# Kernel tuning notes

Hardware: AMD Instinct MI355X
Metric: run time of the kernel (lower is better)

Reference implementation:

```python
import jax, jax.numpy as jnp
import numpy as np

B, T, E = 64, 64, 256
S, ENC = 128, 1024
RNN, ATT, DENSE = 1024, 1024, 8000


def setup_inputs() -> dict:
    key = jax.random.key(0)
    ks = jax.random.split(key, 16)
    s = 0.02
    return {
        "initial_input": jax.random.normal(ks[0], (B, T, E), jnp.float32),
        "hidden": jax.random.normal(ks[1], (B, RNN), jnp.float32),
        "cell": jax.random.normal(ks[2], (B, RNN), jnp.float32),
        "encoder_output": jax.random.normal(ks[3], (B, S, ENC), jnp.float32),
        "W1": jax.random.normal(ks[4], (RNN, ATT), jnp.float32) * s,
        "b1": jnp.zeros((ATT,), jnp.float32),
        "W2": jax.random.normal(ks[5], (ENC, ATT), jnp.float32) * s,
        "b2": jnp.zeros((ATT,), jnp.float32),
        "V": jax.random.normal(ks[6], (ATT, 1), jnp.float32) * s,
        "bV": jnp.zeros((1,), jnp.float32),
        "kernel": jax.random.normal(ks[7], (ENC + E, 4 * RNN), jnp.float32) * s,
        "rkernel": jax.random.normal(ks[8], (RNN, 4 * RNN), jnp.float32) * s,
        "bias": jnp.zeros((4 * RNN,), jnp.float32),
        "Wd": jax.random.normal(ks[9], (RNN, DENSE), jnp.float32) * s,
        "bd": jnp.zeros((DENSE,), jnp.float32),
        "seq_len": T,
    }


def _decode(initial_input, hidden, cell, encoder_output,
            W1, b1, W2, b2, V, bV, kernel, rkernel, bias, Wd, bd):
    # Keys W2(encoder_output) are step-independent: precompute once. [B,S,ATT]
    keys = jnp.einsum('bse,ea->bsa', encoder_output, W2) + b2

    def step(carry, x_t):
        h, c = carry
        # Bahdanau attention: score = V^T tanh(W1 h + W2 enc)
        q = h @ W1 + b1                                  # [B,ATT]
        score = jnp.tanh(q[:, None, :] + keys) @ V + bV   # [B,S,1]
        attn = jax.nn.softmax(score, axis=1)              # [B,S,1]
        ctx = jnp.sum(attn * encoder_output, axis=1)      # [B,ENC]
        # LSTM cell (Keras gate order i,f,g,o; sigmoid/tanh activations)
        inp = jnp.concatenate([ctx, x_t], axis=-1)        # [B,ENC+E]
        z = inp @ kernel + h @ rkernel + bias              # [B,4*RNN]
        i, f, g, o = jnp.split(z, 4, axis=-1)
        i = jax.nn.sigmoid(i)
        f = jax.nn.sigmoid(f)
        g = jnp.tanh(g)
        o = jax.nn.sigmoid(o)
        c_new = f * c + i * g
        h_new = o * jnp.tanh(c_new)
        logits = h_new @ Wd + bd                           # [B,DENSE]
        return (h_new, c_new), logits

    xs = jnp.swapaxes(initial_input, 0, 1)  # [T,B,E]
    (h, c), logits = jax.lax.scan(step, (hidden, cell), xs)
    outputs = jnp.swapaxes(logits, 0, 1)    # [B,T,DENSE]
    return outputs, h, c


def reference(initial_input, hidden, cell, encoder_output,
              W1, b1, W2, b2, V, bV, kernel, rkernel, bias, Wd, bd, seq_len):
    # seq_len == initial_input.shape[1] (static); the Python loop in the
    # original is expressed as an efficient lax.scan over decode steps.
    return _decode(initial_input[:, :seq_len, :], hidden, cell, encoder_output,
                   W1, b1, W2, b2, V, bV, kernel, rkernel, bias, Wd, bd)
```

## Files before the change

### kernel.cpp

```cpp
#include <hip/hip_runtime.h>
#include <hip/hip_bf16.h>
#include <stdint.h>


typedef __attribute__((ext_vector_type(8))) short short8;
typedef __attribute__((ext_vector_type(4))) float floatx4;
typedef __attribute__((ext_vector_type(4))) unsigned short ushortx4;

__device__ __forceinline__ float b2f(unsigned short u) {
    union { unsigned int i; float f; } v; v.i = ((unsigned int)u) << 16; return v.f;
}
__device__ __forceinline__ unsigned short f2b(float f) {
    union { float f; unsigned int i; } v; v.f = f;
    unsigned int r = v.i + 0x7fffu + ((v.i >> 16) & 1u);
    return (unsigned short)(r >> 16);
}
__device__ __forceinline__ float ftanh(float x) {
    x = fminf(15.f, fmaxf(-15.f, x));
    float e = __expf(2.f * x);
    return (e - 1.f) * __builtin_amdgcn_rcpf(e + 1.f);
}
__device__ __forceinline__ float fsig(float x) {
    return __builtin_amdgcn_rcpf(1.f + __expf(-x));
}
__device__ __forceinline__ void ld_lds16(const void* g, void* l) {
    __builtin_amdgcn_global_load_lds((const __attribute__((address_space(1))) void*)g,
                                     (__attribute__((address_space(3))) void*)l, 16, 0, 0);
}

__global__ __launch_bounds__(256) void conv_f32_bf16(
    const float* __restrict__ src, unsigned short* __restrict__ dst, int n4)
{
    int i = blockIdx.x * 256 + threadIdx.x;
    if (i < n4) {
        float4 v = ((const float4*)src)[i];
        ushortx4 o;
        o[0] = f2b(v.x); o[1] = f2b(v.y); o[2] = f2b(v.z); o[3] = f2b(v.w);
        ((ushortx4*)dst)[i] = o;
    }
}

__global__ __launch_bounds__(256) void transpose_conv(
    const float* __restrict__ src, int srcld,
    unsigned short* __restrict__ dst, int dstld, int coloff, int perm)
{
    __shared__ float tile[32][33];
    const int k0 = blockIdx.y * 32, n0 = blockIdx.x * 32;
    const int r = threadIdx.x >> 3, c = (threadIdx.x & 7) * 4;
    int n = n0 + c;
    int cn = perm ? ((((n >> 4) & 3) << 10) | ((n >> 6) << 4) | (n & 15)) : n;
    float4 v = *(const float4*)&src[(size_t)(k0 + r) * srcld + cn];
    tile[r][c + 0] = v.x; tile[r][c + 1] = v.y;
    tile[r][c + 2] = v.z; tile[r][c + 3] = v.w;
    __syncthreads();
    const int nr = threadIdx.x >> 3, kc = (threadIdx.x & 7) * 4;
    ushortx4 o;
    o[0] = f2b(tile[kc + 0][nr]);
    o[1] = f2b(tile[kc + 1][nr]);
    o[2] = f2b(tile[kc + 2][nr]);
    o[3] = f2b(tile[kc + 3][nr]);
    *(ushortx4*)&dst[(size_t)(n0 + nr) * dstld + coloff + k0 + kc] = o;
}

__global__ __launch_bounds__(256) void gemm_bf16_128(
    const unsigned short* __restrict__ A, int lda,
    const unsigned short* __restrict__ BT, int ldbt, int K,
    float* __restrict__ Cf, unsigned short* __restrict__ Cb,
    int ldc, int ncols, const float* __restrict__ bias)
{
    __shared__ __align__(16) unsigned short As[128 * 32];
    __shared__ __align__(16) unsigned short Bs[128 * 32];
    const int tid = threadIdx.x, wave = tid >> 6, lane = tid & 63;
    const int q = lane >> 4, lm = lane & 15;
    const int wr = wave >> 1, wc = wave & 1;
    const int m0 = blockIdx.y * 128, n0 = blockIdx.x * 128;
    const int srow = lane >> 2;
    const int gch = (lane & 3) ^ ((lane >> 3) & 3);
    const unsigned short* Ag0 = A + (size_t)(m0 + wave * 32 + srow) * lda + gch * 8;
    const unsigned short* Ag1 = Ag0 + (size_t)16 * lda;
    const unsigned short* Bg0 = BT + (size_t)(n0 + wave * 32 + srow) * ldbt + gch * 8;
    const unsigned short* Bg1 = Bg0 + (size_t)16 * ldbt;
    unsigned short* Al0 = &As[(wave * 32) * 32];
    unsigned short* Al1 = &As[(wave * 32 + 16) * 32];
    unsigned short* Bl0 = &Bs[(wave * 32) * 32];
    unsigned short* Bl1 = &Bs[(wave * 32 + 16) * 32];

    const floatx4 z4 = {0.f, 0.f, 0.f, 0.f};
    floatx4 acc[4][4];
#pragma unroll
    for (int i = 0; i < 4; i++)
#pragma unroll
        for (int j = 0; j < 4; j++) acc[i][j] = z4;
    const int ach = ((q ^ ((lm >> 1) & 3))) * 8;

    for (int kb = 0; kb < K; kb += 32) {
        ld_lds16(Ag0 + kb, Al0);
        ld_lds16(Ag1 + kb, Al1);
        ld_lds16(Bg0 + kb, Bl0);
        ld_lds16(Bg1 + kb, Bl1);
        __syncthreads();
        short8 a[4], b[4];
#pragma unroll
        for (int i = 0; i < 4; i++) a[i] = *(const short8*)&As[(wr * 64 + i * 16 + lm) * 32 + ach];
#pragma unroll
        for (int j = 0; j < 4; j++) b[j] = *(const short8*)&Bs[(wc * 64 + j * 16 + lm) * 32 + ach];
#pragma unroll
        for (int i = 0; i < 4; i++)
#pragma unroll
            for (int j = 0; j < 4; j++)
                acc[i][j] = __builtin_amdgcn_mfma_f32_16x16x32_bf16(a[i], b[j], acc[i][j], 0, 0, 0);
        __syncthreads();
    }
    const int rb = m0 + wr * 64 + q * 4;
#pragma unroll
    for (int i = 0; i < 4; i++) {
#pragma unroll
        for (int j = 0; j < 4; j++) {
            int col = n0 + wc * 64 + j * 16 + lm;
            if (col < ncols) {
                float bv = bias ? bias[col] : 0.f;
#pragma unroll
                for (int r = 0; r < 4; r++) {
                    float v = acc[i][j][r] + bv;
                    size_t idx = (size_t)(rb + i * 16 + r) * ldc + col;
                    if (Cf) Cf[idx] = v;
                    if (Cb) Cb[idx] = f2b(v);
                }
            }
        }
    }
}

__global__ __launch_bounds__(256) void gemm64_split(
    const unsigned short* __restrict__ A, int lda,
    const unsigned short* __restrict__ BT, int ldbt,
    int kchunk, float* __restrict__ Cpart, int ldc)
{
    __shared__ __align__(16) unsigned short As[4][64 * 32];
    __shared__ __align__(16) unsigned short Bs[4][64 * 32];
    const int tid = threadIdx.x, wave = tid >> 6, lane = tid & 63;
    const int q = lane >> 4, lm = lane & 15;
    const int n0 = blockIdx.x * 64;
    const int k0 = blockIdx.z * kchunk;
    const int srow = lane >> 2;
    const int gch = (lane & 3) ^ ((lane >> 3) & 3);
    const unsigned short* Ag = A + (size_t)(wave * 16 + srow) * lda + k0 + gch * 8;
    const unsigned short* Bg = BT + (size_t)(n0 + wave * 16 + srow) * ldbt + k0 + gch * 8;
    const int loff = (wave * 16) * 32;
    const floatx4 z4 = {0.f, 0.f, 0.f, 0.f};
    floatx4 acc0 = z4, acc1 = z4, acc2 = z4, acc3 = z4;
    const int ach = ((q ^ ((lm >> 1) & 3))) * 8;
    const int nit = kchunk >> 5;

#pragma unroll
    for (int p = 0; p < 3; ++p) {
        if (p < nit) {
            ld_lds16(Ag + p * 32, &As[p][loff]);
            ld_lds16(Bg + p * 32, &Bs[p][loff]);
        }
    }
    for (int it = 0; it < nit; ++it) {
        const int st = it & 3;
        if (it + 2 < nit)      asm volatile("s_waitcnt vmcnt(4)\n\ts_barrier" ::: "memory");
        else if (it + 1 < nit) asm volatile("s_waitcnt vmcnt(2)\n\ts_barrier" ::: "memory");
        else                   asm volatile("s_waitcnt vmcnt(0)\n\ts_barrier" ::: "memory");
        if (it + 3 < nit) {
            const int sn = (it + 3) & 3;
            ld_lds16(Ag + (it + 3) * 32, &As[sn][loff]);
            ld_lds16(Bg + (it + 3) * 32, &Bs[sn][loff]);
        }
        short8 a  = *(const short8*)&As[st][(wave * 16 + lm) * 32 + ach];
        short8 b0 = *(const short8*)&Bs[st][(0 * 16 + lm) * 32 + ach];
        short8 b1 = *(const short8*)&Bs[st][(1 * 16 + lm) * 32 + ach];
        short8 b2 = *(const short8*)&Bs[st][(2 * 16 + lm) * 32 + ach];
        short8 b3 = *(const short8*)&Bs[st][(3 * 16 + lm) * 32 + ach];
        acc0 = __builtin_amdgcn_mfma_f32_16x16x32_bf16(a, b0, acc0, 0, 0, 0);
        acc1 = __builtin_amdgcn_mfma_f32_16x16x32_bf16(a, b1, acc1, 0, 0, 0);
        acc2 = __builtin_amdgcn_mfma_f32_16x16x32_bf16(a, b2, acc2, 0, 0, 0);
        acc3 = __builtin_amdgcn_mfma_f32_16x16x32_bf16(a, b3, acc3, 0, 0, 0);
    }
    float* Cp = Cpart + (size_t)blockIdx.z * 64 * ldc;
    const int rb = wave * 16 + q * 4;
    floatx4 accs[4] = {acc0, acc1, acc2, acc3};
#pragma unroll
    for (int i = 0; i < 4; i++) {
        int col = n0 + i * 16 + lm;
#pragma unroll
        for (int r = 0; r < 4; r++) Cp[(size_t)(rb + r) * ldc + col] = accs[i][r];
    }
}

__global__ __launch_bounds__(256) void init_hc(
    const float* __restrict__ hidden, const float* __restrict__ cell,
    float* __restrict__ hf, float* __restrict__ cb, unsigned short* __restrict__ hbf)
{
    int idx = blockIdx.x * 256 + threadIdx.x;
    float h = hidden[idx], c = cell[idx];
    hf[idx] = h; cb[idx] = c; hbf[idx] = f2b(h);
}

__global__ __launch_bounds__(256) void attn_scores(
    const float* __restrict__ qp, const float* __restrict__ b1,
    const unsigned short* __restrict__ keys,
    const float* __restrict__ V, const float* __restrict__ bV,
    float* __restrict__ sc)
{
    __shared__ float qs[1024];
    __shared__ float vs[1024];
    const int b = blockIdx.y, sg = blockIdx.x;
    const int tid = threadIdx.x, wave = tid >> 6, lane = tid & 63;
    {
        float4 a0 = ((const float4*)(qp + (size_t)b * 1024))[tid];
        float4 a1 = ((const float4*)(qp + 65536 + (size_t)b * 1024))[tid];
        float4 a2 = ((const float4*)(qp + 131072 + (size_t)b * 1024))[tid];
        float4 a3 = ((const float4*)(qp + 196608 + (size_t)b * 1024))[tid];
        float4 ab = ((const float4*)b1)[tid];
        float4 av = ((const float4*)V)[tid];
        float4 r;
        r.x = a0.x + a1.x + a2.x + a3.x + ab.x;
        r.y = a0.y + a1.y + a2.y + a3.y + ab.y;
        r.z = a0.z + a1.z + a2.z + a3.z + ab.z;
        r.w = a0.w + a1.w + a2.w + a3.w + ab.w;
        *(float4*)&qs[tid * 4] = r;
        *(float4*)&vs[tid * 4] = av;
    }
    __syncthreads();
    float qr[16], vr[16];
#pragma unroll
    for (int i = 0; i < 4; i++) {
        float4 tq = *(const float4*)&qs[lane * 16 + i * 4];
        float4 tv = *(const float4*)&vs[lane * 16 + i * 4];
        qr[i * 4 + 0] = tq.x; qr[i * 4 + 1] = tq.y; qr[i * 4 + 2] = tq.z; qr[i * 4 + 3] = tq.w;
        vr[i * 4 + 0] = tv.x; vr[i * 4 + 1] = tv.y; vr[i * 4 + 2] = tv.z; vr[i * 4 + 3] = tv.w;
    }
    const float bv0 = bV[0];
#pragma unroll
    for (int i = 0; i < 4; i++) {
        const int s = sg * 16 + wave * 4 + i;
        const uint4* kp = (const uint4*)(keys + ((size_t)(b * 128 + s)) * 1024 + lane * 16);
        uint4 k0 = kp[0], k1 = kp[1];
        float kf[16];
        kf[0] = b2f((unsigned short)(k0.x & 0xffff)); kf[1] = b2f((unsigned short)(k0.x >> 16));
        kf[2] = b2f((unsigned short)(k0.y & 0xffff)); kf[3] = b2f((unsigned short)(k0.y >> 16));
        kf[4] = b2f((unsigned short)(k0.z & 0xffff)); kf[5] = b2f((unsigned short)(k0.z >> 16));
        kf[6] = b2f((unsigned short)(k0.w & 0xffff)); kf[7] = b2f((unsigned short)(k0.w >> 16));
        kf[8] = b2f((unsigned short)(k1.x & 0xffff)); kf[9] = b2f((unsigned short)(k1.x >> 16));
        kf[10] = b2f((unsigned short)(k1.y & 0xffff)); kf[11] = b2f((unsigned short)(k1.y >> 16));
        kf[12] = b2f((unsigned short)(k1.z & 0xffff)); kf[13] = b2f((unsigned short)(k1.z >> 16));
        kf[14] = b2f((unsigned short)(k1.w & 0xffff)); kf[15] = b2f((unsigned short)(k1.w >> 16));
        float part = 0.f;
#pragma unroll
        for (int j = 0; j < 16; j++) part += vr[j] * ftanh(qr[j] + kf[j]);
#pragma unroll
        for (int off = 32; off; off >>= 1) part += __shfl_xor(part, off);
        if (lane == 0) sc[b * 128 + s] = part + bv0;
    }
}

__global__ __launch_bounds__(256) void softmax_ctx(
    const float* __restrict__ sc, const unsigned short* __restrict__ enc_bf,
    const float* __restrict__ x, const unsigned short* __restrict__ hbf,
    unsigned short* __restrict__ Axc, int t)
{
    __shared__ float attnv[128];
    __shared__ float red[4][64][2];
    __shared__ float smax_s, ssum_s;
    const int b = blockIdx.y, chunk = blockIdx.x;
    const int tid = threadIdx.x, wave = tid >> 6, lane = tid & 63;
    float sv = 0.f;
    if (tid < 128) { sv = sc[b * 128 + tid]; attnv[tid] = sv; }
    __syncthreads();
    if (tid < 64) {
        float m = fmaxf(attnv[tid], attnv[tid + 64]);
#pragma unroll
        for (int off = 32; off; off >>= 1) m = fmaxf(m, __shfl_xor(m, off));
        if (tid == 0) smax_s = m;
    }
    __syncthreads();
    if (tid < 128) attnv[tid] = __expf(sv - smax_s);
    __syncthreads();
    if (tid < 64) {
        float s2 = attnv[tid] + attnv[tid + 64];
#pragma unroll
        for (int off = 32; off; off >>= 1) s2 += __shfl_xor(s2, off);
        if (tid == 0) ssum_s = s2;
    }
    if (chunk < 2 && tid < 64) {
        int c2 = chunk * 128 + tid * 2;
        float x0 = x[((size_t)b * 64 + t) * 256 + c2];
        float x1 = x[((size_t)b * 64 + t) * 256 + c2 + 1];
        *(unsigned int*)&Axc[b * 2304 + 1024 + c2] =
            (unsigned int)f2b(x0) | ((unsigned int)f2b(x1) << 16);
    }
    if (tid < 64) {
        int c2 = chunk * 128 + tid * 2;
        *(unsigned int*)&Axc[b * 2304 + 1280 + c2] =
            *(const unsigned int*)&hbf[b * 1024 + c2];
    }
    const unsigned int* ep = (const unsigned int*)enc_bf + (size_t)b * 65536 + chunk * 64 + lane;
    __syncthreads();
    float ax = 0.f, ay = 0.f;
#pragma unroll 8
    for (int i = 0; i < 32; i++) {
        int s = wave * 32 + i;
        float a = attnv[s];
        unsigned int u = ep[(size_t)s * 512];
        ax += a * b2f((unsigned short)(u & 0xffff));
        ay += a * b2f((unsigned short)(u >> 16));
    }
    red[wave][lane][0] = ax; red[wave][lane][1] = ay;
    __syncthreads();
    if (tid < 64) {
        float rs = __builtin_amdgcn_rcpf(ssum_s);
        float fx = (red[0][lane][0] + red[1][lane][0] + red[2][lane][0] + red[3][lane][0]) * rs;
        float fy = (red[0][lane][1] + red[1][lane][1] + red[2][lane][1] + red[3][lane][1]) * rs;
        *(unsigned int*)&Axc[b * 2304 + chunk * 128 + lane * 2] =
            (unsigned int)f2b(fx) | ((unsigned int)f2b(fy) << 16);
    }
}

__global__ __launch_bounds__(512) void gemm_gates(
    const unsigned short* __restrict__ Axc,
    const unsigned short* __restrict__ KRT,
    const float* __restrict__ bz,
    float* __restrict__ cb, float* __restrict__ hf,
    unsigned short* __restrict__ hbf, unsigned short* __restrict__ Hall, int t)
{
    __shared__ __align__(16) char smem[65536];
    unsigned short* As = (unsigned short*)smem;
    unsigned short* Bs = (unsigned short*)(smem + 32768);
    float* red = (float*)smem;
    const int tid = threadIdx.x, wave = tid >> 6, lane = tid & 63;
    const int q = lane >> 4, lm = lane & 15;
    const int h = wave >> 2, wm = wave & 3;
    const int bx = blockIdx.x;
    const int srow = lane >> 2;
    const int gch = (lane & 3) ^ ((lane >> 3) & 3);
    const unsigned short* Ag = Axc + (size_t)(wm * 16 + srow) * 2304 + h * 1152 + gch * 8;
    const unsigned short* Bg = KRT + (size_t)(bx * 64 + wm * 16 + srow) * 2304 + h * 1152 + gch * 8;
    const int tileoff = h * 2048;
    const int ldoff = tileoff + (wm * 16) * 32;
    const floatx4 z4 = {0.f, 0.f, 0.f, 0.f};
    floatx4 acc0 = z4, acc1 = z4, acc2 = z4, acc3 = z4;
    const int ach = ((q ^ ((lm >> 1) & 3))) * 8;

#pragma unroll
    for (int p = 0; p < 3; ++p) {
        ld_lds16(Ag + p * 32, &As[p * 4096 + ldoff]);
        ld_lds16(Bg + p * 32, &Bs[p * 4096 + ldoff]);
    }
    for (int it = 0; it < 36; ++it) {
        const int st = it & 3;
        if (it < 34)       asm volatile("s_waitcnt vmcnt(4)\n\ts_barrier" ::: "memory");
        else if (it == 34) asm volatile("s_waitcnt vmcnt(2)\n\ts_barrier" ::: "memory");
        else               asm volatile("s_waitcnt vmcnt(0)\n\ts_barrier" ::: "memory");
        if (it + 3 < 36) {
            const int sn = (it + 3) & 3;
            ld_lds16(Ag + (it + 3) * 32, &As[sn * 4096 + ldoff]);
            ld_lds16(Bg + (it + 3) * 32, &Bs[sn * 4096 + ldoff]);
        }
        const unsigned short* Ast = &As[st * 4096 + tileoff];
        const unsigned short* Bst = &Bs[st * 4096 + tileoff];
        short8 a  = *(const short8*)&Ast[(wm * 16 + lm) * 32 + ach];
        short8 b0 = *(const short8*)&Bst[(0 * 16 + lm) * 32 + ach];
        short8 b1 = *(const short8*)&Bst[(1 * 16 + lm) * 32 + ach];
        short8 b2 = *(const short8*)&Bst[(2 * 16 + lm) * 32 + ach];
        short8 b3 = *(const short8*)&Bst[(3 * 16 + lm) * 32 + ach];
        acc0 = __builtin_amdgcn_mfma_f32_16x16x32_bf16(a, b0, acc0, 0, 0, 0);
        acc1 = __builtin_amdgcn_mfma_f32_16x16x32_bf16(a, b1, acc1, 0, 0, 0);
        acc2 = __builtin_amdgcn_mfma_f32_16x16x32_bf16(a, b2, acc2, 0, 0, 0);
        acc3 = __builtin_amdgcn_mfma_f32_16x16x32_bf16(a, b3, acc3, 0, 0, 0);
    }
    __syncthreads();
    if (h == 1) {
        float* rp = &red[(wm * 64 + lane) * 16];
        *(floatx4*)&rp[0]  = acc0; *(floatx4*)&rp[4]  = acc1;
        *(floatx4*)&rp[8]  = acc2; *(floatx4*)&rp[12] = acc3;
    }
    __syncthreads();
    if (h == 0) {
        const float* rp = &red[(wm * 64 + lane) * 16];
        acc0 += *(const floatx4*)&rp[0];
        acc1 += *(const floatx4*)&rp[4];
        acc2 += *(const floatx4*)&rp[8];
        acc3 += *(const floatx4*)&rp[12];
        const int col = bx * 16 + lm;
        const float bzi = bz[col], bzf = bz[1024 + col];
        const float bzg = bz[2048 + col], bzo = bz[3072 + col];
#pragma unroll
        for (int r = 0; r < 4; ++r) {
            const int b = wm * 16 + q * 4 + r;
            float zi = acc0[r] + bzi;
            float zf = acc1[r] + bzf;
            float zg = acc2[r] + bzg;
            float zo = acc3[r] + bzo;
            float ii = fsig(zi), ff = fsig(zf), gg = ftanh(zg), oo = fsig(zo);
            const int idx = b * 1024 + col;
            float cn = ff * cb[idx] + ii * gg;
            float hn = oo * ftanh(cn);
            cb[idx] = cn; hf[idx] = hn;
            unsigned short hb = f2b(hn);
            hbf[idx] = hb;
            Hall[((size_t)b * 64 + t) * 1024 + col] = hb;
        }
    }
}

__global__ __launch_bounds__(256) void tail_k(
    const float* __restrict__ hf, const float* __restrict__ cb, float* __restrict__ out)
{
    int i = blockIdx.x * 256 + threadIdx.x;
    if (i < 65536) out[32768000 + i] = hf[i];
    else out[32768000 + i] = cb[i - 65536];
}

extern "C" void kernel_launch(void* const* d_in, const int* in_sizes, int n_in,
                              void* d_out, int out_size, void* d_ws, size_t ws_size,
                              hipStream_t stream)
{
    const float* x      = (const float*)d_in[0];
    const float* hidden = (const float*)d_in[1];
    const float* cell   = (const float*)d_in[2];
    const float* enc    = (const float*)d_in[3];
    const float* W1     = (const float*)d_in[4];
    const float* b1     = (const float*)d_in[5];
    const float* W2     = (const float*)d_in[6];
    const float* b2     = (const float*)d_in[7];
    const float* V      = (const float*)d_in[8];
    const float* bV     = (const float*)d_in[9];
    const float* Wk     = (const float*)d_in[10];
    const float* rk     = (const float*)d_in[11];
    const float* bz     = (const float*)d_in[12];
    const float* Wd     = (const float*)d_in[13];
    const float* bd     = (const float*)d_in[14];
    float* out = (float*)d_out;

    char* ws = (char*)d_ws;
    unsigned short* enc_bf  = (unsigned short*)(ws + 0);
    unsigned short* keys_bf = (unsigned short*)(ws + 16777216);
    unsigned short* W1T     = (unsigned short*)(ws + 33554432);
    unsigned short* KRT     = (unsigned short*)(ws + 35651584);
    unsigned short* WdT     = (unsigned short*)(ws + 54525952);
    unsigned short* Hall    = (unsigned short*)(ws + 71041024);
    unsigned short* W2T     = Hall;
    unsigned short* Axc     = (unsigned short*)(ws + 79429632);
    float* qp    = (float*)(ws + 79724544);
    float* scbuf = (float*)(ws + 80773120);
    unsigned short* hbf     = (unsigned short*)(ws + 80805888);
    float* hf    = (float*)(ws + 80936960);
    float* cb    = (float*)(ws + 81199104);

    conv_f32_bf16<<<8192, 256, 0, stream>>>(enc, enc_bf, 8388608 / 4);
    transpose_conv<<<dim3(32, 32),  256, 0, stream>>>(W2, 1024, W2T, 1024, 0, 0);
    transpose_conv<<<dim3(32, 32),  256, 0, stream>>>(W1, 1024, W1T, 1024, 0, 0);
    transpose_conv<<<dim3(128, 32), 256, 0, stream>>>(Wk, 4096, KRT, 2304, 0, 1);
    transpose_conv<<<dim3(128, 8),  256, 0, stream>>>(Wk + 1024 * 4096, 4096, KRT, 2304, 1024, 1);
    transpose_conv<<<dim3(128, 32), 256, 0, stream>>>(rk, 4096, KRT, 2304, 1280, 1);
    transpose_conv<<<dim3(250, 32), 256, 0, stream>>>(Wd, 8000, WdT, 1024, 0, 0);
    init_hc<<<256, 256, 0, stream>>>(hidden, cell, hf, cb, hbf);

    gemm_bf16_128<<<dim3(8, 64), 256, 0, stream>>>(enc_bf, 1024, W2T, 1024, 1024,
                                                   nullptr, keys_bf, 1024, 1024, b2);

    for (int t = 0; t < 64; t++) {
        gemm64_split<<<dim3(16, 1, 4), 256, 0, stream>>>(hbf, 1024, W1T, 1024, 256, qp, 1024);
        attn_scores<<<dim3(8, 64), 256, 0, stream>>>(qp, b1, keys_bf, V, bV, scbuf);
        softmax_ctx<<<dim3(8, 64), 256, 0, stream>>>(scbuf, enc_bf, x, hbf, Axc, t);
        gemm_gates<<<64, 512, 0, stream>>>(Axc, KRT, bz, cb, hf, hbf, Hall, t);
    }

    gemm_bf16_128<<<dim3(63, 32), 256, 0, stream>>>(Hall, 1024, WdT, 1024, 1024,
                                                    out, nullptr, 8000, 8000, bd);
    tail_k<<<512, 256, 0, stream>>>(hf, cb, out);
}
```

Before: 2.372 ms.

## Merge prep kernels, fold final state write, swizzle output GEMM, cheaper tanh

Replaces the separate conversion, transpose and init launches with one prep_all kernel indexed by block ID, so there are fewer launches. The final h/c write moves into the last gates step, which removes the tail kernel and the hf buffer. The output GEMM gets an XCD-aware block swizzle so tiles sharing the same A rows land on the same chiplet cache, and its grid grows to 64 columns (relying on the existing ncols guard). The attention tanh switches to a 1-2/(e+1) form with no clamp, which saves a few instructions but could change how extreme inputs are handled.

New measurement: 2.344 ms. No clear change (-1.2%).

```diff
diff --git a/kernel.cpp b/kernel.cpp
--- a/kernel.cpp
+++ b/kernel.cpp
@@ -20,6 +20,9 @@
     float e = __expf(2.f * x);
     return (e - 1.f) * __builtin_amdgcn_rcpf(e + 1.f);
 }
+__device__ __forceinline__ float vtanh(float x) {
+    return __builtin_fmaf(-2.f, __builtin_amdgcn_rcpf(__expf(2.f * x) + 1.f), 1.f);
+}
 __device__ __forceinline__ float fsig(float x) {
     return __builtin_amdgcn_rcpf(1.f + __expf(-x));
 }
@@ -28,32 +31,20 @@
                                      (__attribute__((address_space(3))) void*)l, 16, 0, 0);
 }
 
-__global__ __launch_bounds__(256) void conv_f32_bf16(
-    const float* __restrict__ src, unsigned short* __restrict__ dst, int n4)
-{
-    int i = blockIdx.x * 256 + threadIdx.x;
-    if (i < n4) {
-        float4 v = ((const float4*)src)[i];
-        ushortx4 o;
-        o[0] = f2b(v.x); o[1] = f2b(v.y); o[2] = f2b(v.z); o[3] = f2b(v.w);
-        ((ushortx4*)dst)[i] = o;
-    }
-}
-
-__global__ __launch_bounds__(256) void transpose_conv(
-    const float* __restrict__ src, int srcld,
-    unsigned short* __restrict__ dst, int dstld, int coloff, int perm)
-{
-    __shared__ float tile[32][33];
-    const int k0 = blockIdx.y * 32, n0 = blockIdx.x * 32;
-    const int r = threadIdx.x >> 3, c = (threadIdx.x & 7) * 4;
+__device__ __forceinline__ void tr_tile(
+    float (*tile)[33], const float* __restrict__ src, int srcld,
+    unsigned short* __restrict__ dst, int dstld, int coloff, int perm,
+    int bx, int by, int tid)
+{
+    const int k0 = by * 32, n0 = bx * 32;
+    const int r = tid >> 3, c = (tid & 7) * 4;
     int n = n0 + c;
     int cn = perm ? ((((n >> 4) & 3) << 10) | ((n >> 6) << 4) | (n & 15)) : n;
     float4 v = *(const float4*)&src[(size_t)(k0 + r) * srcld + cn];
     tile[r][c + 0] = v.x; tile[r][c + 1] = v.y;
     tile[r][c + 2] = v.z; tile[r][c + 3] = v.w;
     __syncthreads();
-    const int nr = threadIdx.x >> 3, kc = (threadIdx.x & 7) * 4;
+    const int nr = tid >> 3, kc = (tid & 7) * 4;
     ushortx4 o;
     o[0] = f2b(tile[kc + 0][nr]);
     o[1] = f2b(tile[kc + 1][nr]);
@@ -62,18 +53,67 @@
     *(ushortx4*)&dst[(size_t)(n0 + nr) * dstld + coloff + k0 + kc] = o;
 }
 
+__global__ __launch_bounds__(256) void prep_all(
+    const float* __restrict__ W2, unsigned short* __restrict__ W2T,
+    const float* __restrict__ W1, unsigned short* __restrict__ W1T,
+    const float* __restrict__ Wk, const float* __restrict__ rk,
+    unsigned short* __restrict__ KRT,
+    const float* __restrict__ Wd, unsigned short* __restrict__ WdT,
+    const float* __restrict__ enc, unsigned short* __restrict__ enc_bf,
+    const float* __restrict__ hidden, const float* __restrict__ cell,
+    float* __restrict__ cb, unsigned short* __restrict__ hbf)
+{
+    __shared__ float tile[32][33];
+    const int lid = blockIdx.x, tid = threadIdx.x;
+    if (lid < 1024) {
+        tr_tile(tile, W2, 1024, W2T, 1024, 0, 0, lid & 31, lid >> 5, tid);
+    } else if (lid < 2048) {
+        int l = lid - 1024;
+        tr_tile(tile, W1, 1024, W1T, 1024, 0, 0, l & 31, l >> 5, tid);
+    } else if (lid < 6144) {
+        int l = lid - 2048;
+        tr_tile(tile, Wk, 4096, KRT, 2304, 0, 1, l & 127, l >> 7, tid);
+    } else if (lid < 7168) {
+        int l = lid - 6144;
+        tr_tile(tile, Wk + 1024 * 4096, 4096, KRT, 2304, 1024, 1, l & 127, l >> 7, tid);
+    } else if (lid < 11264) {
+        int l = lid - 7168;
+        tr_tile(tile, rk, 4096, KRT, 2304, 1280, 1, l & 127, l >> 7, tid);
+    } else if (lid < 19264) {
+        int l = lid - 11264;
+        tr_tile(tile, Wd, 8000, WdT, 1024, 0, 0, l % 250, l / 250, tid);
+    } else if (lid < 27456) {
+        int i = (lid - 19264) * 256 + tid;
+        float4 v = ((const float4*)enc)[i];
+        ushortx4 o;
+        o[0] = f2b(v.x); o[1] = f2b(v.y); o[2] = f2b(v.z); o[3] = f2b(v.w);
+        ((ushortx4*)enc_bf)[i] = o;
+    } else {
+        int idx = (lid - 27456) * 256 + tid;
+        float h = hidden[idx], c = cell[idx];
+        cb[idx] = c; hbf[idx] = f2b(h);
+    }
+}
+
 __global__ __launch_bounds__(256) void gemm_bf16_128(
     const unsigned short* __restrict__ A, int lda,
     const unsigned short* __restrict__ BT, int ldbt, int K,
     float* __restrict__ Cf, unsigned short* __restrict__ Cb,
-    int ldc, int ncols, const float* __restrict__ bias)
+    int ldc, int ncols, const float* __restrict__ bias, int swz)
 {
     __shared__ __align__(16) unsigned short As[128 * 32];
     __shared__ __align__(16) unsigned short Bs[128 * 32];
     const int tid = threadIdx.x, wave = tid >> 6, lane = tid & 63;
     const int q = lane >> 4, lm = lane & 15;
     const int wr = wave >> 1, wc = wave & 1;
-    const int m0 = blockIdx.y * 128, n0 = blockIdx.x * 128;
+    int bx = blockIdx.x, by = blockIdx.y;
+    if (swz) {
+        int bid = by * gridDim.x + bx;
+        int xcd = bid & 7, l = bid >> 3;
+        bx = xcd * 8 + (l & 7);
+        by = l >> 3;
+    }
+    const int m0 = by * 128, n0 = bx * 128;
     const int srow = lane >> 2;
     const int gch = (lane & 3) ^ ((lane >> 3) & 3);
     const unsigned short* Ag0 = A + (size_t)(m0 + wave * 32 + srow) * lda + gch * 8;
@@ -190,15 +230,6 @@
     }
 }
 
-__global__ __launch_bounds__(256) void init_hc(
-    const float* __restrict__ hidden, const float* __restrict__ cell,
-    float* __restrict__ hf, float* __restrict__ cb, unsigned short* __restrict__ hbf)
-{
-    int idx = blockIdx.x * 256 + threadIdx.x;
-    float h = hidden[idx], c = cell[idx];
-    hf[idx] = h; cb[idx] = c; hbf[idx] = f2b(h);
-}
-
 __global__ __launch_bounds__(256) void attn_scores(
     const float* __restrict__ qp, const float* __restrict__ b1,
     const unsigned short* __restrict__ keys,
@@ -250,7 +281,7 @@
         kf[14] = b2f((unsigned short)(k1.w & 0xffff)); kf[15] = b2f((unsigned short)(k1.w >> 16));
         float part = 0.f;
 #pragma unroll
-        for (int j = 0; j < 16; j++) part += vr[j] * ftanh(qr[j] + kf[j]);
+        for (int j = 0; j < 16; j++) part += vr[j] * vtanh(qr[j] + kf[j]);
 #pragma unroll
         for (int off = 32; off; off >>= 1) part += __shfl_xor(part, off);
         if (lane == 0) sc[b * 128 + s] = part + bv0;
@@ -323,8 +354,9 @@
     const unsigned short* __restrict__ Axc,
     const unsigned short* __restrict__ KRT,
     const float* __restrict__ bz,
-    float* __restrict__ cb, float* __restrict__ hf,
-    unsigned short* __restrict__ hbf, unsigned short* __restrict__ Hall, int t)
+    float* __restrict__ cb,
+    unsigned short* __restrict__ hbf, unsigned short* __restrict__ Hall, int t,
+    float* __restrict__ out, int last)
 {
     __shared__ __align__(16) char smem[65536];
     unsigned short* As = (unsigned short*)smem;
@@ -398,20 +430,16 @@
             const int idx = b * 1024 + col;
             float cn = ff * cb[idx] + ii * gg;
             float hn = oo * ftanh(cn);
-            cb[idx] = cn; hf[idx] = hn;
+            cb[idx] = cn;
             unsigned short hb = f2b(hn);
             hbf[idx] = hb;
             Hall[((size_t)b * 64 + t) * 1024 + col] = hb;
+            if (last) {
+                out[32768000 + idx] = hn;
+                out[32768000 + 65536 + idx] = cn;
+            }
         }
     }
-}
-
-__global__ __launch_bounds__(256) void tail_k(
-    const float* __restrict__ hf, const float* __restrict__ cb, float* __restrict__ out)
-{
-    int i = blockIdx.x * 256 + threadIdx.x;
-    if (i < 65536) out[32768000 + i] = hf[i];
-    else out[32768000 + i] = cb[i - 65536];
 }
 
 extern "C" void kernel_launch(void* const* d_in, const int* in_sizes, int n_in,
@@ -441,35 +469,28 @@
     unsigned short* W1T     = (unsigned short*)(ws + 33554432);
     unsigned short* KRT     = (unsigned short*)(ws + 35651584);
     unsigned short* WdT     = (unsigned short*)(ws + 54525952);
-    unsigned short* Hall    = (unsigned short*)(ws + 71041024);
+    unsigned short* Hall    = (unsigned short*)(ws + 71303168);
     unsigned short* W2T     = Hall;
-    unsigned short* Axc     = (unsigned short*)(ws + 79429632);
-    float* qp    = (float*)(ws + 79724544);
-    float* scbuf = (float*)(ws + 80773120);
-    unsigned short* hbf     = (unsigned short*)(ws + 80805888);
-    float* hf    = (float*)(ws + 80936960);
+    unsigned short* Axc     = (unsigned short*)(ws + 79691776);
+    float* qp    = (float*)(ws + 79986688);
+    unsigned short* hbf     = (unsigned short*)(ws + 81035264);
+    float* scbuf = (float*)(ws + 81166336);
     float* cb    = (float*)(ws + 81199104);
 
-    conv_f32_bf16<<<8192, 256, 0, stream>>>(enc, enc_bf, 8388608 / 4);
-    transpose_conv<<<dim3(32, 32),  256, 0, stream>>>(W2, 1024, W2T, 1024, 0, 0);
-    transpose_conv<<<dim3(32, 32),  256, 0, stream>>>(W1, 1024, W1T, 1024, 0, 0);
-    transpose_conv<<<dim3(128, 32), 256, 0, stream>>>(Wk, 4096, KRT, 2304, 0, 1);
-    transpose_conv<<<dim3(128, 8),  256, 0, stream>>>(Wk + 1024 * 4096, 4096, KRT, 2304, 1024, 1);
-    transpose_conv<<<dim3(128, 32), 256, 0, stream>>>(rk, 4096, KRT, 2304, 1280, 1);
-    transpose_conv<<<dim3(250, 32), 256, 0, stream>>>(Wd, 8000, WdT, 1024, 0, 0);
-    init_hc<<<256, 256, 0, stream>>>(hidden, cell, hf, cb, hbf);
+    prep_all<<<27712, 256, 0, stream>>>(W2, W2T, W1, W1T, Wk, rk, KRT, Wd, WdT,
+                                        enc, enc_bf, hidden, cell, cb, hbf);
 
     gemm_bf16_128<<<dim3(8, 64), 256, 0, stream>>>(enc_bf, 1024, W2T, 1024, 1024,
-                                                   nullptr, keys_bf, 1024, 1024, b2);
+                                                   nullptr, keys_bf, 1024, 1024, b2, 0);
 
     for (int t = 0; t < 64; t++) {
         gemm64_split<<<dim3(16, 1, 4), 256, 0, stream>>>(hbf, 1024, W1T, 1024, 256, qp, 1024);
         attn_scores<<<dim3(8, 64), 256, 0, stream>>>(qp, b1, keys_bf, V, bV, scbuf);
         softmax_ctx<<<dim3(8, 64), 256, 0, stream>>>(scbuf, enc_bf, x, hbf, Axc, t);
-        gemm_gates<<<64, 512, 0, stream>>>(Axc, KRT, bz, cb, hf, hbf, Hall, t);
-    }
-
-    gemm_bf16_128<<<dim3(63, 32), 256, 0, stream>>>(Hall, 1024, WdT, 1024, 1024,
-                                                    out, nullptr, 8000, 8000, bd);
-    tail_k<<<512, 256, 0, stream>>>(hf, cb, out);
-}
+        gemm_gates<<<64, 512, 0, stream>>>(Axc, KRT, bz, cb, hbf, Hall, t,
+                                           out, (t == 63) ? 1 : 0);
+    }
+
+    gemm_bf16_128<<<dim3(64, 32), 256, 0, stream>>>(Hall, 1024, WdT, 1024, 1024,
+                                                    out, nullptr, 8000, 8000, bd, 1);
+}
```
